# Performance work log

Hardware: AMD Instinct MI355X
Metric: run time of the kernel (lower is better)

The kernel has to match this reference:

```python
import jax, jax.numpy as jnp
import numpy as np

N_NODES = 100_000
N_EDGES = 800_000
HIDDEN = 150
EDGE_FEAT = 7
N_LAYERS = 4
N_GRAPHS = 128
OUT_DIM = 6
BN_EPS = 1e-5


def setup_inputs() -> dict:
    key = jax.random.key(0)
    ks = jax.random.split(key, 16)
    x = jnp.zeros((N_NODES,), dtype=jnp.int32)  # Embedding(1, D) -> all indices 0
    edge_index = jax.random.randint(ks[0], (2, N_EDGES), 0, N_NODES, dtype=jnp.int32)
    edge_attr = jax.random.normal(ks[1], (N_EDGES, EDGE_FEAT), dtype=jnp.float32)
    batch = jnp.sort(jax.random.randint(ks[2], (N_NODES,), 0, N_GRAPHS, dtype=jnp.int32))
    s = 0.05
    node_emb = jax.random.normal(ks[3], (1, HIDDEN), dtype=jnp.float32) * s
    Wl = jax.random.normal(ks[4], (N_LAYERS, HIDDEN, HIDDEN), dtype=jnp.float32) * s
    bl = jnp.zeros((N_LAYERS, HIDDEN), dtype=jnp.float32)
    We = jax.random.normal(ks[5], (N_LAYERS, EDGE_FEAT, HIDDEN), dtype=jnp.float32) * s
    be = jnp.zeros((N_LAYERS, HIDDEN), dtype=jnp.float32)
    root = jax.random.normal(ks[6], (N_LAYERS, 1, HIDDEN), dtype=jnp.float32) * s
    gamma = jnp.ones((N_LAYERS, HIDDEN), dtype=jnp.float32)
    beta = jnp.zeros((N_LAYERS, HIDDEN), dtype=jnp.float32)
    Wp = jax.random.normal(ks[7], (HIDDEN, OUT_DIM), dtype=jnp.float32) * s
    bp = jnp.zeros((OUT_DIM,), dtype=jnp.float32)
    return {"x": x, "edge_index": edge_index, "edge_attr": edge_attr, "batch": batch,
            "node_emb": node_emb, "Wl": Wl, "bl": bl, "We": We, "be": be,
            "root": root, "gamma": gamma, "beta": beta, "Wp": Wp, "bp": bp}


def reference(x, edge_index, edge_attr, batch, node_emb, Wl, bl, We, be, root, gamma, beta, Wp, bp):
    n = x.shape[0]
    row, col = edge_index[0], edge_index[1]  # j=source, i=target (PyG default flow)
    # degree over row (as in GCNConv.forward), +1
    deg = jax.ops.segment_sum(jnp.ones((row.shape[0],), edge_attr.dtype), row, num_segments=n) + 1.0
    dis = deg ** -0.5  # deg >= 1, no inf
    norm = dis[row] * dis[col]  # [E]

    h = node_emb[x]  # [N, D]
    for l in range(N_LAYERS):
        xl = h @ Wl[l] + bl[l]                      # linear
        e = edge_attr @ We[l] + be[l]               # edge encoder
        msg = norm[:, None] * jax.nn.relu(xl[row] + e)      # per-edge message [E, D]
        agg = jax.ops.segment_sum(msg, col, num_segments=n)  # scatter-add to targets
        out = agg + jax.nn.relu(xl + root[l]) / deg[:, None]
        # BatchNorm1d (training-mode batch statistics; dropout disabled = eval)
        mu = out.mean(axis=0)
        var = out.var(axis=0)
        out = gamma[l] * (out - mu) * jax.lax.rsqrt(var + BN_EPS) + beta[l]
        if l < N_LAYERS - 1:
            out = jax.nn.relu(out)
        h = out + h  # residual=True

    # global mean pool over graphs
    counts = jax.ops.segment_sum(jnp.ones((n,), h.dtype), batch, num_segments=N_GRAPHS)
    hg = jax.ops.segment_sum(h, batch, num_segments=N_GRAPHS) / jnp.maximum(counts, 1.0)[:, None]
    return hg @ Wp + bp  # [G, OUT_DIM]
```

## Files before the change

kernel.cpp:

```cpp
#include <hip/hip_runtime.h>

#define HID 150
#define LD  160
#define NN  100000
#define NNP 100096
#define NE  800000
#define NG  128
#define NL  4
#define ODIM 6
#define BN_EPS 1e-5f
#define NSLICE 32
#define NB_SCAN 98

typedef __attribute__((ext_vector_type(8))) short short8;
typedef __attribute__((ext_vector_type(4))) float f32x4;

__device__ __forceinline__ unsigned short f2bf(float f) {
    union { float f; unsigned int u; } v; v.f = f;
    unsigned int u = v.u;
    unsigned int r = (u + 0x7FFFu + ((u >> 16) & 1u)) >> 16;
    return (unsigned short)r;
}
__device__ __forceinline__ float bf2f(unsigned short h) {
    union { unsigned int u; float f; } v; v.u = ((unsigned int)h) << 16;
    return v.f;
}

#if defined(__has_builtin)
#if __has_builtin(__builtin_amdgcn_fdot2_f32_bf16)
#define HAS_DOT2BF 1
#endif
#endif
#ifdef HAS_DOT2BF
typedef __attribute__((ext_vector_type(2))) __bf16 bf16x2;
#endif
__device__ __forceinline__ float dot2bf(unsigned int a, unsigned int b, float c) {
#ifdef HAS_DOT2BF
    union { unsigned int u; bf16x2 v; } ua, ub;
    ua.u = a; ub.u = b;
    return __builtin_amdgcn_fdot2_f32_bf16(ua.v, ub.v, c, false);
#else
    return fmaf(bf2f((unsigned short)(a & 0xffffu)), bf2f((unsigned short)(b & 0xffffu)),
           fmaf(bf2f((unsigned short)(a >> 16)), bf2f((unsigned short)(b >> 16)), c));
#endif
}

__global__ __launch_bounds__(256) void k_deg_count(const int* __restrict__ erow,
                                                   const int* __restrict__ ecol,
                                                   int* __restrict__ degi,
                                                   int* __restrict__ indeg) {
    int e = blockIdx.x * 256 + threadIdx.x;
    if (e < NE) {
        atomicAdd(&degi[erow[e]], 1);
        atomicAdd(&indeg[ecol[e]], 1);
    }
}

__global__ __launch_bounds__(256) void k_deg_fin(const int* __restrict__ degi,
                                                 float* __restrict__ degf,
                                                 float* __restrict__ dis) {
    int n = blockIdx.x * 256 + threadIdx.x;
    if (n < NN) {
        float dg = (float)degi[n] + 1.0f;
        degf[n] = dg;
        dis[n] = rsqrtf(dg);
    }
}

__global__ __launch_bounds__(1024) void k_scanA(const int* __restrict__ in,
                                                int* __restrict__ part,
                                                int* __restrict__ btot) {
    const int tid = threadIdx.x;
    const int lane = tid & 63, wave = tid >> 6;
    const int i = blockIdx.x * 1024 + tid;
    int v = (i < NN) ? in[i] : 0;
    int x = v;
#pragma unroll
    for (int o = 1; o < 64; o <<= 1) {
        int t = __shfl_up(x, o);
        if (lane >= o) x += t;
    }
    __shared__ int wsum[16];
    __shared__ int blocktot;
    if (lane == 63) wsum[wave] = x;
    __syncthreads();
    if (tid < 16) {
        int t = wsum[tid];
        int y = t;
#pragma unroll
        for (int o = 1; o < 16; o <<= 1) {
            int u = __shfl_up(y, o);
            if (tid >= o) y += u;
        }
        wsum[tid] = y - t;
        if (tid == 15) blocktot = y;
    }
    __syncthreads();
    int excl = x - v + wsum[wave];
    if (i < NN) part[i] = excl;
    if (tid == 0) btot[blockIdx.x] = blocktot;
}

__global__ __launch_bounds__(128) void k_scanB(int* __restrict__ btot) {
    const int tid = threadIdx.x;
    const int lane = tid & 63;
    int v = (tid < NB_SCAN) ? btot[tid] : 0;
    int x = v;
#pragma unroll
    for (int o = 1; o < 64; o <<= 1) {
        int t = __shfl_up(x, o);
        if (lane >= o) x += t;
    }
    __shared__ int w2;
    if (tid == 63) w2 = x;
    __syncthreads();
    int ex = x - v + ((tid >= 64) ? w2 : 0);
    if (tid < NB_SCAN) btot[tid] = ex;
}

__global__ __launch_bounds__(256) void k_scanC(int* __restrict__ coff,
                                               const int* __restrict__ btot,
                                               int* __restrict__ cursor) {
    int i = blockIdx.x * 256 + threadIdx.x;
    if (i < NN) {
        int v = coff[i] + btot[i >> 10];
        coff[i] = v;
        cursor[i] = v;
    }
    if (i == 0) coff[NN] = NE;
}

__global__ __launch_bounds__(256) void k_csr_fill(const int* __restrict__ erow,
                                                  const int* __restrict__ ecol,
                                                  const float* __restrict__ ea,
                                                  const float* __restrict__ dis,
                                                  int* __restrict__ cursor,
                                                  int2* __restrict__ csrn,
                                                  uint4* __restrict__ ceab) {
    int e = blockIdx.x * 256 + threadIdx.x;
    if (e >= NE) return;
    const int c = ecol[e], r = erow[e];
    const int p = atomicAdd(&cursor[c], 1);
    int2 m; m.x = r; m.y = __float_as_int(dis[r] * dis[c]);
    csrn[p] = m;
    const float a0 = ea[e * 7 + 0], a1 = ea[e * 7 + 1], a2 = ea[e * 7 + 2],
                a3 = ea[e * 7 + 3], a4 = ea[e * 7 + 4], a5 = ea[e * 7 + 5],
                a6 = ea[e * 7 + 6];
    uint4 A;
    A.x = (unsigned)f2bf(a0) | ((unsigned)f2bf(a1) << 16);
    A.y = (unsigned)f2bf(a2) | ((unsigned)f2bf(a3) << 16);
    A.z = (unsigned)f2bf(a4) | ((unsigned)f2bf(a5) << 16);
    A.w = (unsigned)f2bf(a6);
    ceab[p] = A;
}

__global__ __launch_bounds__(256) void k_wpack(const float* __restrict__ Wl,
                                               unsigned short* __restrict__ Wp) {
    int t = blockIdx.x * 256 + threadIdx.x;
    if (t >= 12800) return;
    const int lane = t & 63;
    const int ct = (t >> 6) % 10;
    const int ks = ((t >> 6) / 10) % 5;
    const int l = t / (64 * 10 * 5);
    const int col = ct * 16 + (lane & 15);
    const int kbase = ks * 32 + (lane >> 4) * 8;
    unsigned short v[8];
#pragma unroll
    for (int j = 0; j < 8; ++j) {
        const int k = kbase + j;
        const float f = (k < HID && col < HID) ? Wl[(size_t)l * HID * HID + k * HID + col] : 0.f;
        v[j] = f2bf(f);
    }
    *(uint4*)(Wp + (size_t)t * 8) = *(const uint4*)v;
}

__global__ __launch_bounds__(256) void k_init_h(const int* __restrict__ x,
                                                const float* __restrict__ emb,
                                                float* __restrict__ h) {
    int idx = blockIdx.x * 256 + threadIdx.x;
    if (idx >= NNP * LD) return;
    int n = idx / LD;
    int d = idx - n * LD;
    float v = 0.f;
    if (n < NN && d < HID) v = emb[x[n] * HID + d];
    h[idx] = v;
}

__global__ __launch_bounds__(256) void k_gemm(float* __restrict__ h,
                                              const float* __restrict__ obuf,
                                              const float* __restrict__ ssb,
                                              const unsigned short* __restrict__ Wp,
                                              const float* __restrict__ bias,
                                              unsigned short* __restrict__ xlb,
                                              int fuse) {
    __shared__ unsigned short Bs[5 * 10 * 64 * 8];
    {
        const uint4* src = (const uint4*)Wp;
        uint4* dst = (uint4*)Bs;
        for (int i = threadIdx.x; i < 3200; i += 256) dst[i] = src[i];
    }
    __syncthreads();

    const int wave = threadIdx.x >> 6;
    const int lane = threadIdx.x & 63;
    const int row0 = (blockIdx.x * 4 + wave) * 16;
    const int rlo = lane & 15;
    const int khi = lane >> 4;
    const int row = row0 + rlo;
    const bool rowok = row < NN;

    short8 a[5];
    if (fuse) {
#pragma unroll
        for (int ks = 0; ks < 5; ++ks) {
            const int kf = ks * 32 + khi * 8;
            const size_t base = (size_t)row * LD + kf;
            const float4 o0 = *(const float4*)(obuf + base);
            const float4 o1 = *(const float4*)(obuf + base + 4);
            const float4 h0 = *(const float4*)(h + base);
            const float4 h1 = *(const float4*)(h + base + 4);
            const float4 s0 = *(const float4*)(ssb + kf);
            const float4 s1 = *(const float4*)(ssb + kf + 4);
            const float4 t0 = *(const float4*)(ssb + LD + kf);
            const float4 t1 = *(const float4*)(ssb + LD + kf + 4);
            float hv[8];
#pragma unroll
            for (int j = 0; j < 4; ++j) {
                const bool ok = rowok && (kf + j < HID);
                hv[j] = ok ? ((&h0.x)[j] + fmaxf((&o0.x)[j] * (&s0.x)[j] + (&t0.x)[j], 0.f)) : 0.f;
            }
#pragma unroll
            for (int j = 0; j < 4; ++j) {
                const bool ok = rowok && (kf + 4 + j < HID);
                hv[4 + j] = ok ? ((&h1.x)[j] + fmaxf((&o1.x)[j] * (&s1.x)[j] + (&t1.x)[j], 0.f)) : 0.f;
            }
            float4 w0, w1;
            w0.x = hv[0]; w0.y = hv[1]; w0.z = hv[2]; w0.w = hv[3];
            w1.x = hv[4]; w1.y = hv[5]; w1.z = hv[6]; w1.w = hv[7];
            *(float4*)(h + base) = w0;
            *(float4*)(h + base + 4) = w1;
            short8 av;
#pragma unroll
            for (int j = 0; j < 8; ++j) av[j] = (short)f2bf(hv[j]);
            a[ks] = av;
        }
    } else {
#pragma unroll
        for (int ks = 0; ks < 5; ++ks) {
            const int kf = ks * 32 + khi * 8;
            const size_t base = (size_t)row * LD + kf;
            const float4 h0 = *(const float4*)(h + base);
            const float4 h1 = *(const float4*)(h + base + 4);
            short8 av;
#pragma unroll
            for (int j = 0; j < 4; ++j) av[j] = (short)f2bf((&h0.x)[j]);
#pragma unroll
            for (int j = 0; j < 4; ++j) av[4 + j] = (short)f2bf((&h1.x)[j]);
            a[ks] = av;
        }
    }

    f32x4 acc[10];
#pragma unroll
    for (int ct = 0; ct < 10; ++ct) acc[ct] = (f32x4){0.f, 0.f, 0.f, 0.f};

    const short8* bs = (const short8*)Bs;
#pragma unroll
    for (int ks = 0; ks < 5; ++ks) {
#pragma unroll
        for (int ct = 0; ct < 10; ++ct) {
            acc[ct] = __builtin_amdgcn_mfma_f32_16x16x32_bf16(
                a[ks], bs[(ks * 10 + ct) * 64 + lane], acc[ct], 0, 0, 0);
        }
    }

#pragma unroll
    for (int ct = 0; ct < 10; ++ct) {
        const int col = ct * 16 + rlo;
        if (col < HID) {
            const float b = bias[col];
#pragma unroll
            for (int jj = 0; jj < 4; ++jj) {
                const int orow = row0 + khi * 4 + jj;
                xlb[(size_t)orow * LD + col] = f2bf(acc[ct][jj] + b);
            }
        }
    }
}

__global__ __launch_bounds__(256) void k_agg(const int* __restrict__ coff,
                                             const int2* __restrict__ csrn,
                                             const uint4* __restrict__ ceab,
                                             const float* __restrict__ We,
                                             const float* __restrict__ be,
                                             const float* __restrict__ root,
                                             const float* __restrict__ degf,
                                             const unsigned short* __restrict__ xlb,
                                             float* __restrict__ out,
                                             float* __restrict__ sums) {
    const int lane = threadIdx.x & 63;
    const int gw = (blockIdx.x * 256 + threadIdx.x) >> 6;
    const int nw = (gridDim.x * 256) >> 6;
    const bool ok2 = lane < (HID - 128);
    const int d0 = lane, d1 = lane + 64;
    const int d2 = ok2 ? (lane + 128) : 0;

    unsigned int wp0[4], wp1[4], wp2[4];
    float be0, be1, be2, rt0, rt1, rt2;
    {
#pragma unroll
        for (int p = 0; p < 3; ++p) {
            wp0[p] = (unsigned)f2bf(We[(2 * p) * HID + d0]) | ((unsigned)f2bf(We[(2 * p + 1) * HID + d0]) << 16);
            wp1[p] = (unsigned)f2bf(We[(2 * p) * HID + d1]) | ((unsigned)f2bf(We[(2 * p + 1) * HID + d1]) << 16);
            wp2[p] = ok2 ? ((unsigned)f2bf(We[(2 * p) * HID + d2]) | ((unsigned)f2bf(We[(2 * p + 1) * HID + d2]) << 16)) : 0u;
        }
        wp0[3] = (unsigned)f2bf(We[6 * HID + d0]);
        wp1[3] = (unsigned)f2bf(We[6 * HID + d1]);
        wp2[3] = ok2 ? (unsigned)f2bf(We[6 * HID + d2]) : 0u;
        be0 = be[d0]; be1 = be[d1]; be2 = ok2 ? be[d2] : 0.f;
        rt0 = root[d0]; rt1 = root[d1]; rt2 = ok2 ? root[d2] : 0.f;
    }

    float s0 = 0.f, s1 = 0.f, s2 = 0.f, q0 = 0.f, q1 = 0.f, q2 = 0.f;

#define ACC_EDGE(m, A, xa, xb, xc)                                                          \
    do {                                                                                    \
        const float nrm = __int_as_float((m).y);                                            \
        const float e0 = dot2bf((A).x, wp0[0], dot2bf((A).y, wp0[1],                        \
                         dot2bf((A).z, wp0[2], dot2bf((A).w, wp0[3], be0))));               \
        const float e1 = dot2bf((A).x, wp1[0], dot2bf((A).y, wp1[1],                        \
                         dot2bf((A).z, wp1[2], dot2bf((A).w, wp1[3], be1))));               \
        acc0 += nrm * fmaxf(bf2f(xa) + e0, 0.f);                                            \
        acc1 += nrm * fmaxf(bf2f(xb) + e1, 0.f);                                            \
        if (ok2) {                                                                          \
            const float e2 = dot2bf((A).x, wp2[0], dot2bf((A).y, wp2[1],                    \
                             dot2bf((A).z, wp2[2], dot2bf((A).w, wp2[3], be2))));           \
            acc2 += nrm * fmaxf(bf2f(xc) + e2, 0.f);                                        \
        }                                                                                   \
    } while (0)

    for (int i = gw; i < NN; i += nw) {
        const int j1 = coff[i + 1];
        int j = coff[i];
        float acc0 = 0.f, acc1 = 0.f, acc2 = 0.f;
        for (; j + 4 <= j1; j += 4) {
            const int2 m0 = csrn[j], m1 = csrn[j + 1], m2 = csrn[j + 2], m3 = csrn[j + 3];
            const uint4 A0 = ceab[j], A1 = ceab[j + 1], A2 = ceab[j + 2], A3 = ceab[j + 3];
            const unsigned short* p0 = xlb + (size_t)m0.x * LD;
            const unsigned short* p1 = xlb + (size_t)m1.x * LD;
            const unsigned short* p2 = xlb + (size_t)m2.x * LD;
            const unsigned short* p3 = xlb + (size_t)m3.x * LD;
            const unsigned short x0a = p0[d0], x0b = p0[d1], x0c = p0[d2];
            const unsigned short x1a = p1[d0], x1b = p1[d1], x1c = p1[d2];
            const unsigned short x2a = p2[d0], x2b = p2[d1], x2c = p2[d2];
            const unsigned short x3a = p3[d0], x3b = p3[d1], x3c = p3[d2];
            ACC_EDGE(m0, A0, x0a, x0b, x0c);
            ACC_EDGE(m1, A1, x1a, x1b, x1c);
            ACC_EDGE(m2, A2, x2a, x2b, x2c);
            ACC_EDGE(m3, A3, x3a, x3b, x3c);
        }
        for (; j < j1; ++j) {
            const int2 m0 = csrn[j];
            const uint4 A0 = ceab[j];
            const unsigned short* p0 = xlb + (size_t)m0.x * LD;
            const unsigned short x0a = p0[d0], x0b = p0[d1], x0c = p0[d2];
            ACC_EDGE(m0, A0, x0a, x0b, x0c);
        }

        const float inv = 1.0f / degf[i];
        const unsigned short* xi = xlb + (size_t)i * LD;
        float* op = out + (size_t)i * LD;
        {
            const float o = acc0 + fmaxf(bf2f(xi[d0]) + rt0, 0.f) * inv;
            op[d0] = o; s0 += o; q0 += o * o;
        }
        {
            const float o = acc1 + fmaxf(bf2f(xi[d1]) + rt1, 0.f) * inv;
            op[d1] = o; s1 += o; q1 += o * o;
        }
        if (ok2) {
            const float o = acc2 + fmaxf(bf2f(xi[d2]) + rt2, 0.f) * inv;
            op[d2] = o; s2 += o; q2 += o * o;
        }
    }
#undef ACC_EDGE

    __shared__ float ls[2 * LD];
    for (int i = threadIdx.x; i < 2 * LD; i += 256) ls[i] = 0.f;
    __syncthreads();
    atomicAdd(&ls[d0], s0);
    atomicAdd(&ls[LD + d0], q0);
    atomicAdd(&ls[d1], s1);
    atomicAdd(&ls[LD + d1], q1);
    if (ok2) {
        atomicAdd(&ls[d2], s2);
        atomicAdd(&ls[LD + d2], q2);
    }
    __syncthreads();
    float* sl = sums + (size_t)(blockIdx.x & (NSLICE - 1)) * 2 * LD;
    for (int i = threadIdx.x; i < 2 * LD; i += 256) atomicAdd(&sl[i], ls[i]);
}

__global__ void k_stats(const float* __restrict__ sums, const float* __restrict__ gamma,
                        const float* __restrict__ beta, float* __restrict__ ss) {
    int d = threadIdx.x;
    if (d < HID) {
        float s = 0.f, q = 0.f;
        for (int r = 0; r < NSLICE; ++r) {
            s += sums[r * 2 * LD + d];
            q += sums[r * 2 * LD + LD + d];
        }
        const float mu = s * (1.0f / NN);
        const float var = q * (1.0f / NN) - mu * mu;
        const float inv = rsqrtf(var + BN_EPS);
        const float sc = gamma[d] * inv;
        ss[d] = sc;
        ss[LD + d] = beta[d] - mu * sc;
    } else if (d < LD) {
        ss[d] = 0.f;
        ss[LD + d] = 0.f;
    }
}

__global__ __launch_bounds__(256) void k_off(const int* __restrict__ batch,
                                             int* __restrict__ off) {
    int n = blockIdx.x * 256 + threadIdx.x;
    if (n >= NN) return;
    int b = batch[n];
    if (n == 0) {
        for (int g = 0; g <= b; ++g) off[g] = 0;
    } else {
        int pb = batch[n - 1];
        for (int g = pb + 1; g <= b; ++g) off[g] = n;
    }
    if (n == NN - 1) {
        for (int g = b + 1; g <= NG; ++g) off[g] = NN;
    }
}

__global__ __launch_bounds__(512) void k_pool(const float* __restrict__ h,
                                              const float* __restrict__ obuf,
                                              const float* __restrict__ ssb,
                                              const int* __restrict__ off,
                                              const float* __restrict__ Wp,
                                              const float* __restrict__ bp,
                                              float* __restrict__ out) {
    const int g = blockIdx.x;
    const int s = off[g], e = off[g + 1];
    const float cnt = fmaxf((float)(e - s), 1.0f);
    const int lane = threadIdx.x & 63;
    const int wave = threadIdx.x >> 6;
    const bool ok2 = lane < (HID - 128);
    const int d0 = lane, d1 = lane + 64;
    const int d2 = ok2 ? (lane + 128) : 0;

    const float sc0 = ssb[d0], sc1 = ssb[d1], sc2 = ok2 ? ssb[d2] : 0.f;
    const float sh0 = ssb[LD + d0], sh1 = ssb[LD + d1], sh2 = ok2 ? ssb[LD + d2] : 0.f;

    float sum0 = 0.f, sum1 = 0.f, sum2 = 0.f;
    for (int n = s + wave; n < e; n += 8) {
        const float* hp = h + (size_t)n * LD;
        const float* op = obuf + (size_t)n * LD;
        sum0 += hp[d0] + (op[d0] * sc0 + sh0);
        sum1 += hp[d1] + (op[d1] * sc1 + sh1);
        if (ok2) sum2 += hp[d2] + (op[d2] * sc2 + sh2);
    }

    __shared__ float hg[LD];
    if (threadIdx.x < LD) hg[threadIdx.x] = 0.f;
    __syncthreads();
    atomicAdd(&hg[d0], sum0);
    atomicAdd(&hg[d1], sum1);
    if (ok2) atomicAdd(&hg[d2], sum2);
    __syncthreads();

    if (wave == 0) {
        float acc[ODIM] = {0.f, 0.f, 0.f, 0.f, 0.f, 0.f};
#pragma unroll
        for (int c = 0; c < 3; ++c) {
            const int d = c * 64 + lane;
            if (d < HID) {
                const float v = hg[d] / cnt;
#pragma unroll
                for (int o = 0; o < ODIM; ++o) acc[o] = fmaf(v, Wp[d * ODIM + o], acc[o]);
            }
        }
#pragma unroll
        for (int o = 0; o < ODIM; ++o) {
            float v = acc[o];
            for (int sh = 32; sh > 0; sh >>= 1) v += __shfl_down(v, sh);
            if (lane == 0) out[g * ODIM + o] = v + bp[o];
        }
    }
}

extern "C" void kernel_launch(void* const* d_in, const int* in_sizes, int n_in,
                              void* d_out, int out_size, void* d_ws, size_t ws_size,
                              hipStream_t stream) {
    const int* x = (const int*)d_in[0];
    const int* ei = (const int*)d_in[1];
    const float* ea = (const float*)d_in[2];
    const int* batch = (const int*)d_in[3];
    const float* emb = (const float*)d_in[4];
    const float* Wl = (const float*)d_in[5];
    const float* bl = (const float*)d_in[6];
    const float* We = (const float*)d_in[7];
    const float* be = (const float*)d_in[8];
    const float* root = (const float*)d_in[9];
    const float* gamma = (const float*)d_in[10];
    const float* beta = (const float*)d_in[11];
    const float* Wp = (const float*)d_in[12];
    const float* bp = (const float*)d_in[13];
    float* out = (float*)d_out;

    const int* erow = ei;
    const int* ecol = ei + NE;

    char* ws = (char*)d_ws;
    const size_t SZ4 = (size_t)NNP * LD * 4;
    const size_t SZ2 = (size_t)NNP * LD * 2;
    float* h    = (float*)(ws);
    float* obuf = (float*)(ws + SZ4);
    unsigned short* xlb = (unsigned short*)(ws + 2 * SZ4);
    unsigned short* wpk = (unsigned short*)(ws + 2 * SZ4 + SZ2);
    char* base = ws + 2 * SZ4 + SZ2 + 204800;
    int*   degi   = (int*)(base);
    int*   indeg  = (int*)(base + 409600);
    float* degf   = (float*)(base + 819200);
    float* dis    = (float*)(base + 1228800);
    int*   coff   = (int*)(base + 1638400);
    int*   cursor = (int*)(base + 2048000);
    int*   btot   = (int*)(base + 2457600);
    float* sums   = (float*)(base + 2461696);
    float* ssb    = (float*)(base + 2502656);
    int*   goff   = (int*)(base + 2506752);
    int2*  csrn   = (int2*)(base + 2510848);
    uint4* ceab   = (uint4*)(base + 8910848);

    hipMemsetAsync(degi, 0, NN * sizeof(int), stream);
    hipMemsetAsync(indeg, 0, NN * sizeof(int), stream);
    k_deg_count<<<(NE + 255) / 256, 256, 0, stream>>>(erow, ecol, degi, indeg);
    k_deg_fin<<<(NN + 255) / 256, 256, 0, stream>>>(degi, degf, dis);
    k_scanA<<<NB_SCAN, 1024, 0, stream>>>(indeg, coff, btot);
    k_scanB<<<1, 128, 0, stream>>>(btot);
    k_scanC<<<(NN + 255) / 256, 256, 0, stream>>>(coff, btot, cursor);
    k_csr_fill<<<(NE + 255) / 256, 256, 0, stream>>>(erow, ecol, ea, dis, cursor,
                                                     csrn, ceab);
    k_wpack<<<50, 256, 0, stream>>>(Wl, wpk);
    k_init_h<<<(NNP * LD + 255) / 256, 256, 0, stream>>>(x, emb, h);

    for (int l = 0; l < NL; ++l) {
        const float* b_l = bl + (size_t)l * HID;
        const float* We_l = We + (size_t)l * 7 * HID;
        const float* be_l = be + (size_t)l * HID;
        const float* root_l = root + (size_t)l * HID;
        const float* gamma_l = gamma + (size_t)l * HID;
        const float* beta_l = beta + (size_t)l * HID;
        const unsigned short* wpk_l = wpk + (size_t)l * 25600;

        k_gemm<<<NNP / 64, 256, 0, stream>>>(h, obuf, ssb, wpk_l, b_l, xlb,
                                             (l > 0) ? 1 : 0);
        hipMemsetAsync(sums, 0, NSLICE * 2 * LD * sizeof(float), stream);
        k_agg<<<2048, 256, 0, stream>>>(coff, csrn, ceab, We_l, be_l,
                                        root_l, degf, xlb, obuf, sums);
        k_stats<<<1, 256, 0, stream>>>(sums, gamma_l, beta_l, ssb);
    }

    k_off<<<(NN + 255) / 256, 256, 0, stream>>>(batch, goff);
    k_pool<<<NG, 512, 0, stream>>>(h, obuf, ssb, goff, Wp, bp, out);
}
```

Measured before the change: 903.8 us.

## Store aggregation output in bf16 and gather two features per lane

The aggregation output buffer changes from fp32 to bf16, which halves its write traffic in k_agg and its read traffic in the fused GEMM prologue and the pooling kernel. k_agg also changes its feature mapping so each lane owns two adjacent features and loads them as one 32-bit word, with 11 lanes covering the 22-feature tail. This cuts the number of gather instructions per edge. The cost is bf16 rounding of the pre-BatchNorm activations, while the statistics are still accumulated from the fp32 values.

Result: faster. 871.4 us (-3.6%).

```diff
diff --git a/kernel.cpp b/kernel.cpp
--- a/kernel.cpp
+++ b/kernel.cpp
@@ -187,7 +187,7 @@
 }
 
 __global__ __launch_bounds__(256) void k_gemm(float* __restrict__ h,
-                                              const float* __restrict__ obuf,
+                                              const unsigned short* __restrict__ obuf,
                                               const float* __restrict__ ssb,
                                               const unsigned short* __restrict__ Wp,
                                               const float* __restrict__ bias,
@@ -215,8 +215,7 @@
         for (int ks = 0; ks < 5; ++ks) {
             const int kf = ks * 32 + khi * 8;
             const size_t base = (size_t)row * LD + kf;
-            const float4 o0 = *(const float4*)(obuf + base);
-            const float4 o1 = *(const float4*)(obuf + base + 4);
+            const short8 ov = *(const short8*)(obuf + base);
             const float4 h0 = *(const float4*)(h + base);
             const float4 h1 = *(const float4*)(h + base + 4);
             const float4 s0 = *(const float4*)(ssb + kf);
@@ -227,12 +226,14 @@
 #pragma unroll
             for (int j = 0; j < 4; ++j) {
                 const bool ok = rowok && (kf + j < HID);
-                hv[j] = ok ? ((&h0.x)[j] + fmaxf((&o0.x)[j] * (&s0.x)[j] + (&t0.x)[j], 0.f)) : 0.f;
+                const float o = bf2f((unsigned short)ov[j]);
+                hv[j] = ok ? ((&h0.x)[j] + fmaxf(o * (&s0.x)[j] + (&t0.x)[j], 0.f)) : 0.f;
             }
 #pragma unroll
             for (int j = 0; j < 4; ++j) {
                 const bool ok = rowok && (kf + 4 + j < HID);
-                hv[4 + j] = ok ? ((&h1.x)[j] + fmaxf((&o1.x)[j] * (&s1.x)[j] + (&t1.x)[j], 0.f)) : 0.f;
+                const float o = bf2f((unsigned short)ov[4 + j]);
+                hv[4 + j] = ok ? ((&h1.x)[j] + fmaxf(o * (&s1.x)[j] + (&t1.x)[j], 0.f)) : 0.f;
             }
             float4 w0, w1;
             w0.x = hv[0]; w0.y = hv[1]; w0.z = hv[2]; w0.w = hv[3];
@@ -296,53 +297,56 @@
                                              const float* __restrict__ root,
                                              const float* __restrict__ degf,
                                              const unsigned short* __restrict__ xlb,
-                                             float* __restrict__ out,
+                                             unsigned short* __restrict__ out,
                                              float* __restrict__ sums) {
     const int lane = threadIdx.x & 63;
     const int gw = (blockIdx.x * 256 + threadIdx.x) >> 6;
     const int nw = (gridDim.x * 256) >> 6;
-    const bool ok2 = lane < (HID - 128);
-    const int d0 = lane, d1 = lane + 64;
-    const int d2 = ok2 ? (lane + 128) : 0;
-
-    unsigned int wp0[4], wp1[4], wp2[4];
-    float be0, be1, be2, rt0, rt1, rt2;
-    {
-#pragma unroll
-        for (int p = 0; p < 3; ++p) {
-            wp0[p] = (unsigned)f2bf(We[(2 * p) * HID + d0]) | ((unsigned)f2bf(We[(2 * p + 1) * HID + d0]) << 16);
-            wp1[p] = (unsigned)f2bf(We[(2 * p) * HID + d1]) | ((unsigned)f2bf(We[(2 * p + 1) * HID + d1]) << 16);
-            wp2[p] = ok2 ? ((unsigned)f2bf(We[(2 * p) * HID + d2]) | ((unsigned)f2bf(We[(2 * p + 1) * HID + d2]) << 16)) : 0u;
-        }
-        wp0[3] = (unsigned)f2bf(We[6 * HID + d0]);
-        wp1[3] = (unsigned)f2bf(We[6 * HID + d1]);
-        wp2[3] = ok2 ? (unsigned)f2bf(We[6 * HID + d2]) : 0u;
-        be0 = be[d0]; be1 = be[d1]; be2 = ok2 ? be[d2] : 0.f;
-        rt0 = root[d0]; rt1 = root[d1]; rt2 = ok2 ? root[d2] : 0.f;
-    }
-
-    float s0 = 0.f, s1 = 0.f, s2 = 0.f, q0 = 0.f, q1 = 0.f, q2 = 0.f;
-
-#define ACC_EDGE(m, A, xa, xb, xc)                                                          \
-    do {                                                                                    \
-        const float nrm = __int_as_float((m).y);                                            \
-        const float e0 = dot2bf((A).x, wp0[0], dot2bf((A).y, wp0[1],                        \
-                         dot2bf((A).z, wp0[2], dot2bf((A).w, wp0[3], be0))));               \
-        const float e1 = dot2bf((A).x, wp1[0], dot2bf((A).y, wp1[1],                        \
-                         dot2bf((A).z, wp1[2], dot2bf((A).w, wp1[3], be1))));               \
-        acc0 += nrm * fmaxf(bf2f(xa) + e0, 0.f);                                            \
-        acc1 += nrm * fmaxf(bf2f(xb) + e1, 0.f);                                            \
-        if (ok2) {                                                                          \
-            const float e2 = dot2bf((A).x, wp2[0], dot2bf((A).y, wp2[1],                    \
-                             dot2bf((A).z, wp2[2], dot2bf((A).w, wp2[3], be2))));           \
-            acc2 += nrm * fmaxf(bf2f(xc) + e2, 0.f);                                        \
-        }                                                                                   \
+    const int f0 = lane * 2;
+    const bool tl = lane < 11;
+    const int ft = tl ? (128 + lane * 2) : 128;
+
+    unsigned wa[4], wb[4], wta[4], wtb[4];
+    float bea, beb, bet0, bet1, rta, rtb, rtt0, rtt1;
+#pragma unroll
+    for (int p = 0; p < 3; ++p) {
+        wa[p] = (unsigned)f2bf(We[(2 * p) * HID + f0]) | ((unsigned)f2bf(We[(2 * p + 1) * HID + f0]) << 16);
+        wb[p] = (unsigned)f2bf(We[(2 * p) * HID + f0 + 1]) | ((unsigned)f2bf(We[(2 * p + 1) * HID + f0 + 1]) << 16);
+        wta[p] = tl ? ((unsigned)f2bf(We[(2 * p) * HID + ft]) | ((unsigned)f2bf(We[(2 * p + 1) * HID + ft]) << 16)) : 0u;
+        wtb[p] = tl ? ((unsigned)f2bf(We[(2 * p) * HID + ft + 1]) | ((unsigned)f2bf(We[(2 * p + 1) * HID + ft + 1]) << 16)) : 0u;
+    }
+    wa[3] = (unsigned)f2bf(We[6 * HID + f0]);
+    wb[3] = (unsigned)f2bf(We[6 * HID + f0 + 1]);
+    wta[3] = tl ? (unsigned)f2bf(We[6 * HID + ft]) : 0u;
+    wtb[3] = tl ? (unsigned)f2bf(We[6 * HID + ft + 1]) : 0u;
+    bea = be[f0]; beb = be[f0 + 1];
+    bet0 = tl ? be[ft] : 0.f; bet1 = tl ? be[ft + 1] : 0.f;
+    rta = root[f0]; rtb = root[f0 + 1];
+    rtt0 = tl ? root[ft] : 0.f; rtt1 = tl ? root[ft + 1] : 0.f;
+
+    float sa = 0.f, sb = 0.f, st0 = 0.f, st1 = 0.f;
+    float qa = 0.f, qb = 0.f, qt0 = 0.f, qt1 = 0.f;
+
+#define ENC(AA, WW, CC) dot2bf((AA).x, (WW)[0], dot2bf((AA).y, (WW)[1], dot2bf((AA).z, (WW)[2], dot2bf((AA).w, (WW)[3], (CC)))))
+#define ACC_EDGE(MM, AA, XM, XT)                                                     \
+    do {                                                                             \
+        const float nrm = __int_as_float((MM).y);                                    \
+        const float e0 = ENC(AA, wa, bea);                                           \
+        const float e1 = ENC(AA, wb, beb);                                           \
+        acc_a += nrm * fmaxf(bf2f((unsigned short)((XM) & 0xffffu)) + e0, 0.f);      \
+        acc_b += nrm * fmaxf(bf2f((unsigned short)((XM) >> 16)) + e1, 0.f);          \
+        if (tl) {                                                                    \
+            const float e2 = ENC(AA, wta, bet0);                                     \
+            const float e3 = ENC(AA, wtb, bet1);                                     \
+            acc_t0 += nrm * fmaxf(bf2f((unsigned short)((XT) & 0xffffu)) + e2, 0.f); \
+            acc_t1 += nrm * fmaxf(bf2f((unsigned short)((XT) >> 16)) + e3, 0.f);     \
+        }                                                                            \
     } while (0)
 
     for (int i = gw; i < NN; i += nw) {
         const int j1 = coff[i + 1];
         int j = coff[i];
-        float acc0 = 0.f, acc1 = 0.f, acc2 = 0.f;
+        float acc_a = 0.f, acc_b = 0.f, acc_t0 = 0.f, acc_t1 = 0.f;
         for (; j + 4 <= j1; j += 4) {
             const int2 m0 = csrn[j], m1 = csrn[j + 1], m2 = csrn[j + 2], m3 = csrn[j + 3];
             const uint4 A0 = ceab[j], A1 = ceab[j + 1], A2 = ceab[j + 2], A3 = ceab[j + 3];
@@ -350,51 +354,61 @@
             const unsigned short* p1 = xlb + (size_t)m1.x * LD;
             const unsigned short* p2 = xlb + (size_t)m2.x * LD;
             const unsigned short* p3 = xlb + (size_t)m3.x * LD;
-            const unsigned short x0a = p0[d0], x0b = p0[d1], x0c = p0[d2];
-            const unsigned short x1a = p1[d0], x1b = p1[d1], x1c = p1[d2];
-            const unsigned short x2a = p2[d0], x2b = p2[d1], x2c = p2[d2];
-            const unsigned short x3a = p3[d0], x3b = p3[d1], x3c = p3[d2];
-            ACC_EDGE(m0, A0, x0a, x0b, x0c);
-            ACC_EDGE(m1, A1, x1a, x1b, x1c);
-            ACC_EDGE(m2, A2, x2a, x2b, x2c);
-            ACC_EDGE(m3, A3, x3a, x3b, x3c);
+            const unsigned x0m = *(const unsigned*)(p0 + f0);
+            const unsigned x1m = *(const unsigned*)(p1 + f0);
+            const unsigned x2m = *(const unsigned*)(p2 + f0);
+            const unsigned x3m = *(const unsigned*)(p3 + f0);
+            const unsigned x0t = tl ? *(const unsigned*)(p0 + ft) : 0u;
+            const unsigned x1t = tl ? *(const unsigned*)(p1 + ft) : 0u;
+            const unsigned x2t = tl ? *(const unsigned*)(p2 + ft) : 0u;
+            const unsigned x3t = tl ? *(const unsigned*)(p3 + ft) : 0u;
+            ACC_EDGE(m0, A0, x0m, x0t);
+            ACC_EDGE(m1, A1, x1m, x1t);
+            ACC_EDGE(m2, A2, x2m, x2t);
+            ACC_EDGE(m3, A3, x3m, x3t);
         }
         for (; j < j1; ++j) {
             const int2 m0 = csrn[j];
             const uint4 A0 = ceab[j];
             const unsigned short* p0 = xlb + (size_t)m0.x * LD;
-            const unsigned short x0a = p0[d0], x0b = p0[d1], x0c = p0[d2];
-            ACC_EDGE(m0, A0, x0a, x0b, x0c);
+            const unsigned x0m = *(const unsigned*)(p0 + f0);
+            const unsigned x0t = tl ? *(const unsigned*)(p0 + ft) : 0u;
+            ACC_EDGE(m0, A0, x0m, x0t);
         }
 
         const float inv = 1.0f / degf[i];
         const unsigned short* xi = xlb + (size_t)i * LD;
-        float* op = out + (size_t)i * LD;
+        unsigned short* op = out + (size_t)i * LD;
+        const unsigned xim = *(const unsigned*)(xi + f0);
+        const unsigned xit = tl ? *(const unsigned*)(xi + ft) : 0u;
         {
-            const float o = acc0 + fmaxf(bf2f(xi[d0]) + rt0, 0.f) * inv;
-            op[d0] = o; s0 += o; q0 += o * o;
-        }
-        {
-            const float o = acc1 + fmaxf(bf2f(xi[d1]) + rt1, 0.f) * inv;
-            op[d1] = o; s1 += o; q1 += o * o;
-        }
-        if (ok2) {
-            const float o = acc2 + fmaxf(bf2f(xi[d2]) + rt2, 0.f) * inv;
-            op[d2] = o; s2 += o; q2 += o * o;
+            const float oa = acc_a + fmaxf(bf2f((unsigned short)(xim & 0xffffu)) + rta, 0.f) * inv;
+            const float ob = acc_b + fmaxf(bf2f((unsigned short)(xim >> 16)) + rtb, 0.f) * inv;
+            *(unsigned*)(op + f0) = (unsigned)f2bf(oa) | ((unsigned)f2bf(ob) << 16);
+            sa += oa; qa += oa * oa; sb += ob; qb += ob * ob;
+        }
+        if (tl) {
+            const float ot0 = acc_t0 + fmaxf(bf2f((unsigned short)(xit & 0xffffu)) + rtt0, 0.f) * inv;
+            const float ot1 = acc_t1 + fmaxf(bf2f((unsigned short)(xit >> 16)) + rtt1, 0.f) * inv;
+            *(unsigned*)(op + ft) = (unsigned)f2bf(ot0) | ((unsigned)f2bf(ot1) << 16);
+            st0 += ot0; qt0 += ot0 * ot0; st1 += ot1; qt1 += ot1 * ot1;
         }
     }
 #undef ACC_EDGE
+#undef ENC
 
     __shared__ float ls[2 * LD];
     for (int i = threadIdx.x; i < 2 * LD; i += 256) ls[i] = 0.f;
     __syncthreads();
-    atomicAdd(&ls[d0], s0);
-    atomicAdd(&ls[LD + d0], q0);
-    atomicAdd(&ls[d1], s1);
-    atomicAdd(&ls[LD + d1], q1);
-    if (ok2) {
-        atomicAdd(&ls[d2], s2);
-        atomicAdd(&ls[LD + d2], q2);
+    atomicAdd(&ls[f0], sa);
+    atomicAdd(&ls[f0 + 1], sb);
+    atomicAdd(&ls[LD + f0], qa);
+    atomicAdd(&ls[LD + f0 + 1], qb);
+    if (tl) {
+        atomicAdd(&ls[ft], st0);
+        atomicAdd(&ls[ft + 1], st1);
+        atomicAdd(&ls[LD + ft], qt0);
+        atomicAdd(&ls[LD + ft + 1], qt1);
     }
     __syncthreads();
     float* sl = sums + (size_t)(blockIdx.x & (NSLICE - 1)) * 2 * LD;
@@ -439,7 +453,7 @@
 }
 
 __global__ __launch_bounds__(512) void k_pool(const float* __restrict__ h,
-                                              const float* __restrict__ obuf,
+                                              const unsigned short* __restrict__ obuf,
                                               const float* __restrict__ ssb,
                                               const int* __restrict__ off,
                                               const float* __restrict__ Wp,
@@ -460,10 +474,10 @@
     float sum0 = 0.f, sum1 = 0.f, sum2 = 0.f;
     for (int n = s + wave; n < e; n += 8) {
         const float* hp = h + (size_t)n * LD;
-        const float* op = obuf + (size_t)n * LD;
-        sum0 += hp[d0] + (op[d0] * sc0 + sh0);
-        sum1 += hp[d1] + (op[d1] * sc1 + sh1);
-        if (ok2) sum2 += hp[d2] + (op[d2] * sc2 + sh2);
+        const unsigned short* op = obuf + (size_t)n * LD;
+        sum0 += hp[d0] + (bf2f(op[d0]) * sc0 + sh0);
+        sum1 += hp[d1] + (bf2f(op[d1]) * sc1 + sh1);
+        if (ok2) sum2 += hp[d2] + (bf2f(op[d2]) * sc2 + sh2);
     }
 
     __shared__ float hg[LD];
@@ -520,10 +534,10 @@
     const size_t SZ4 = (size_t)NNP * LD * 4;
     const size_t SZ2 = (size_t)NNP * LD * 2;
     float* h    = (float*)(ws);
-    float* obuf = (float*)(ws + SZ4);
-    unsigned short* xlb = (unsigned short*)(ws + 2 * SZ4);
-    unsigned short* wpk = (unsigned short*)(ws + 2 * SZ4 + SZ2);
-    char* base = ws + 2 * SZ4 + SZ2 + 204800;
+    unsigned short* xlb  = (unsigned short*)(ws + SZ4);
+    unsigned short* obuf = (unsigned short*)(ws + SZ4 + SZ2);
+    unsigned short* wpk  = (unsigned short*)(ws + SZ4 + 2 * SZ2);
+    char* base = ws + SZ4 + 2 * SZ2 + 204800;
     int*   degi   = (int*)(base);
     int*   indeg  = (int*)(base + 409600);
     float* degf   = (float*)(base + 819200);
```
